# Performance work log

Measured on AMD Instinct MI355X. Metric: run time of the kernel, lower is better.

Reference implementation:

```python
import jax, jax.numpy as jnp
import numpy as np

N_NODES = 100000
N_EDGES = 1600000
N_FEATS = 64
HID1 = 128
HID2 = 128


def setup_inputs() -> dict:
    key = jax.random.key(0)
    ks = jax.random.split(key, 8)
    x = jax.random.normal(ks[0], (N_NODES, N_FEATS), dtype=jnp.float32)
    edge_index = jax.random.randint(ks[1], (2, N_EDGES), 0, N_NODES, dtype=jnp.int64)
    # glorot-ish init for linear weights (out_feats, in_feats), bias zeros (PyG default)
    W1 = jax.random.normal(ks[2], (HID1, N_FEATS), dtype=jnp.float32) * (1.0 / np.sqrt(N_FEATS))
    b1 = jnp.zeros((HID1,), dtype=jnp.float32)
    W2 = jax.random.normal(ks[3], (HID2, HID1), dtype=jnp.float32) * (1.0 / np.sqrt(HID1))
    b2 = jnp.zeros((HID2,), dtype=jnp.float32)
    W3 = jax.random.normal(ks[4], (N_FEATS, HID2), dtype=jnp.float32) * (1.0 / np.sqrt(HID2))
    b3 = jnp.zeros((N_FEATS,), dtype=jnp.float32)
    return {"x": x, "edge_index": edge_index, "W1": W1, "b1": b1,
            "W2": W2, "b2": b2, "W3": W3, "b3": b3}


def _gcn_conv(x, src, dst, norm, W, b, n_nodes):
    # dense linear transform first (out_dim may differ from in_dim)
    h = x @ W.T                                   # [N, out]
    msg = h[src] * norm[:, None]                  # gather + edge-normalize, [E+N, out]
    out = jax.ops.segment_sum(msg, dst, num_segments=n_nodes)  # scatter-add
    return out + b


def reference(x, edge_index, W1, b1, W2, b2, W3, b3):
    n = x.shape[0]
    loop = jnp.arange(n, dtype=edge_index.dtype)
    src = jnp.concatenate([edge_index[0], loop])  # self-loops appended (PyG default)
    dst = jnp.concatenate([edge_index[1], loop])
    # symmetric normalization: deg over target column incl. self-loops
    deg = jax.ops.segment_sum(jnp.ones(dst.shape, dtype=x.dtype), dst, num_segments=n)
    dinv = jnp.where(deg > 0, jax.lax.rsqrt(deg), 0.0)
    norm = dinv[src] * dinv[dst]                  # [E+N]

    h = jax.nn.relu(_gcn_conv(x, src, dst, norm, W1, b1, n))
    h = jax.nn.relu(_gcn_conv(h, src, dst, norm, W2, b2, n))
    h = _gcn_conv(h, src, dst, norm, W3, b3, n)
    return jax.nn.softmax(h, axis=1)
```

## Files before the change

kernel.cpp:

```cpp
#include <hip/hip_runtime.h>
#include <hip/hip_bf16.h>


#define NB1 256

typedef __attribute__((ext_vector_type(4))) _Float16 half4;
typedef __attribute__((ext_vector_type(8))) _Float16 half8;
typedef __attribute__((ext_vector_type(4))) float f32x4;


__global__ __launch_bounds__(256) void k_hist(const int* __restrict__ dst, int E, int C,
                                              int NBUK, int* __restrict__ gh) {
  __shared__ int h[512];
  int t = threadIdx.x, b = blockIdx.x;
  for (int i = t; i < NBUK; i += 256) h[i] = 0;
  __syncthreads();
  int beg = b * C, end = min(beg + C, E);
  for (int i = beg + t; i < end; i += 256) atomicAdd(&h[dst[i] >> 8], 1);
  __syncthreads();
  for (int i = t; i < NBUK; i += 256) gh[i * NB1 + b] = h[i];
}

__global__ __launch_bounds__(256) void k_sum256(const int* __restrict__ g, int L,
                                                int* __restrict__ part) {
  __shared__ int red[256];
  int t = threadIdx.x;
  int idx = blockIdx.x * 256 + t;
  red[t] = (idx < L) ? g[idx] : 0;
  __syncthreads();
  for (int off = 128; off > 0; off >>= 1) {
    if (t < off) red[t] += red[t + off];
    __syncthreads();
  }
  if (t == 0) part[blockIdx.x] = red[0];
}

__global__ __launch_bounds__(512) void k_scan_part(int* __restrict__ part, int NP) {
  __shared__ int sh[512];
  int t = threadIdx.x;
  int v = (t < NP) ? part[t] : 0;
  sh[t] = v;
  __syncthreads();
  for (int off = 1; off < 512; off <<= 1) {
    int u = (t >= off) ? sh[t - off] : 0;
    __syncthreads();
    sh[t] += u;
    __syncthreads();
  }
  if (t < NP) part[t] = sh[t] - v;
}

__global__ __launch_bounds__(256) void k_scan_apply(const int* __restrict__ g, int L,
                                                    const int* __restrict__ part,
                                                    int* __restrict__ gout) {
  __shared__ int sh[256];
  int t = threadIdx.x;
  int idx = blockIdx.x * 256 + t;
  int v = (idx < L) ? g[idx] : 0;
  sh[t] = v;
  __syncthreads();
  for (int off = 1; off < 256; off <<= 1) {
    int u = (t >= off) ? sh[t - off] : 0;
    __syncthreads();
    sh[t] += u;
    __syncthreads();
  }
  if (idx < L) gout[idx] = part[blockIdx.x] + sh[t] - v;
}

__global__ __launch_bounds__(256) void k_scatter(const int* __restrict__ src,
                                                 const int* __restrict__ dst, int E, int C,
                                                 int NBUK, const int* __restrict__ gscan,
                                                 int* __restrict__ epak) {
  __shared__ int cur[512];
  int t = threadIdx.x, b = blockIdx.x;
  for (int i = t; i < NBUK; i += 256) cur[i] = gscan[i * NB1 + b];
  __syncthreads();
  int beg = b * C, end = min(beg + C, E);
  for (int i = beg + t; i < end; i += 256) {
    int d = dst[i];
    int p = atomicAdd(&cur[d >> 8], 1);
    epak[p] = src[i] | ((d & 255) << 24);
  }
}

__global__ __launch_bounds__(256) void k_csr(const int* __restrict__ epak,
                                             const int* __restrict__ gscan, int NBUK, int N, int E,
                                             int* __restrict__ rowptr, float* __restrict__ dinv,
                                             int* __restrict__ col) {
  __shared__ int cnt[256];
  __shared__ int scn[256];
  __shared__ int cur[256];
  int b = blockIdx.x, t = threadIdx.x;
  int ebeg = gscan[b * NB1];
  int eend = (b + 1 < NBUK) ? gscan[(b + 1) * NB1] : E;
  cnt[t] = 0;
  __syncthreads();
  for (int i = ebeg + t; i < eend; i += 256) atomicAdd(&cnt[(epak[i] >> 24) & 255], 1);
  __syncthreads();
  int c = cnt[t];
  scn[t] = c;
  __syncthreads();
  for (int off = 1; off < 256; off <<= 1) {
    int v = (t >= off) ? scn[t - off] : 0;
    __syncthreads();
    scn[t] += v;
    __syncthreads();
  }
  int excl = scn[t] - c;
  int node = b * 256 + t;
  if (node < N) {
    rowptr[node] = ebeg + excl;
    dinv[node] = rsqrtf((float)(c + 1));
  }
  cur[t] = ebeg + excl;
  __syncthreads();
  for (int i = ebeg + t; i < eend; i += 256) {
    int e = epak[i];
    int p = atomicAdd(&cur[(e >> 24) & 255], 1);
    col[p] = e & 0xFFFFFF;
  }
  if (b == 0 && t == 0) rowptr[N] = E;
}

__global__ __launch_bounds__(256) void k_prep_w(const float* __restrict__ W1,
                                                const float* __restrict__ W2,
                                                const float* __restrict__ W3,
                                                _Float16* __restrict__ w1h,
                                                _Float16* __restrict__ w2h,
                                                _Float16* __restrict__ w3h) {
  int i = blockIdx.x * 256 + threadIdx.x;
  if (i < 128 * 64) w1h[i] = (_Float16)W1[i];
  if (i < 128 * 128) w2h[i] = (_Float16)W2[i];
  if (i < 64 * 128) w3h[i] = (_Float16)W3[i];
}

__global__ __launch_bounds__(256) void k_prescaleh(const float* __restrict__ x,
                                                   const float* __restrict__ dinv,
                                                   _Float16* __restrict__ xp, int N) {
  int i = blockIdx.x * 256 + threadIdx.x;
  if (i < N * 16) {
    int row = i >> 4;
    float4 v = ((const float4*)x)[i];
    float d = dinv[row];
    half4 o;
    o[0] = (_Float16)(v.x * d);
    o[1] = (_Float16)(v.y * d);
    o[2] = (_Float16)(v.z * d);
    o[3] = (_Float16)(v.w * d);
    ((half4*)xp)[i] = o;
  }
}


template <int EPI>
__global__ __launch_bounds__(256) void k_agg64h(const _Float16* __restrict__ hp,
                                                const float* __restrict__ dinv,
                                                const int* __restrict__ rowptr,
                                                const int* __restrict__ col,
                                                const float* __restrict__ bias,
                                                void* __restrict__ outp, int N) {
  int wid = blockIdx.x * 4 + (threadIdx.x >> 6);
  int lane = threadIdx.x & 63;
  if (wid >= N) return;
  int g = lane >> 3;
  int fl = (lane & 7) * 8;
  float acc[8] = {0.f, 0.f, 0.f, 0.f, 0.f, 0.f, 0.f, 0.f};
  int r0 = rowptr[wid], r1 = rowptr[wid + 1];
  for (int base = r0; base < r1; base += 64) {
    int mm = min(64, r1 - base);
    int ce = (base + lane < r1) ? col[base + lane] : 0;
    for (int j = 0; j < mm; j += 16) {
      int i0 = j + g, i1 = j + 8 + g;
      int s0 = __shfl(ce, i0);
      int s1 = __shfl(ce, i1);
      if (i0 < mm) {
        half8 v = *(const half8*)&hp[(size_t)s0 * 64 + fl];
#pragma unroll
        for (int k = 0; k < 8; ++k) acc[k] += (float)v[k];
      }
      if (i1 < mm) {
        half8 v = *(const half8*)&hp[(size_t)s1 * 64 + fl];
#pragma unroll
        for (int k = 0; k < 8; ++k) acc[k] += (float)v[k];
      }
    }
  }
#pragma unroll
  for (int o = 8; o < 64; o <<= 1) {
#pragma unroll
    for (int k = 0; k < 8; ++k) acc[k] += __shfl_xor(acc[k], o);
  }
  half8 sv = *(const half8*)&hp[(size_t)wid * 64 + fl];
  float di = dinv[wid];
  float v[8];
#pragma unroll
  for (int k = 0; k < 8; ++k) v[k] = di * (acc[k] + (float)sv[k]);
  if (EPI == 0) {
    if (lane < 8) {
      half8 o;
#pragma unroll
      for (int k = 0; k < 8; ++k) o[k] = (_Float16)v[k];
      *(half8*)&((_Float16*)outp)[(size_t)wid * 64 + fl] = o;
    }
  } else {
    float4 ba = *(const float4*)&bias[fl];
    float4 bb = *(const float4*)&bias[fl + 4];
    v[0] += ba.x; v[1] += ba.y; v[2] += ba.z; v[3] += ba.w;
    v[4] += bb.x; v[5] += bb.y; v[6] += bb.z; v[7] += bb.w;
    float mx = v[0];
#pragma unroll
    for (int k = 1; k < 8; ++k) mx = fmaxf(mx, v[k]);
#pragma unroll
    for (int o = 1; o < 8; o <<= 1) mx = fmaxf(mx, __shfl_xor(mx, o));
    float s = 0.f;
#pragma unroll
    for (int k = 0; k < 8; ++k) {
      v[k] = expf(v[k] - mx);
      s += v[k];
    }
#pragma unroll
    for (int o = 1; o < 8; o <<= 1) s += __shfl_xor(s, o);
    float inv = 1.0f / s;
#pragma unroll
    for (int k = 0; k < 8; ++k) v[k] *= inv;
    if (lane < 8) {
      float4 o0 = make_float4(v[0], v[1], v[2], v[3]);
      float4 o1 = make_float4(v[4], v[5], v[6], v[7]);
      *(float4*)&((float*)outp)[(size_t)wid * 64 + fl] = o0;
      *(float4*)&((float*)outp)[(size_t)wid * 64 + fl + 4] = o1;
    }
  }
}

__global__ __launch_bounds__(256) void k_agg128h(const _Float16* __restrict__ hp,
                                                 const float* __restrict__ dinv,
                                                 const int* __restrict__ rowptr,
                                                 const int* __restrict__ col,
                                                 _Float16* __restrict__ out, int N) {
  int wid = blockIdx.x * 4 + (threadIdx.x >> 6);
  int lane = threadIdx.x & 63;
  if (wid >= N) return;
  int g = lane >> 4;
  int fl = (lane & 15) * 8;
  float acc[8] = {0.f, 0.f, 0.f, 0.f, 0.f, 0.f, 0.f, 0.f};
  int r0 = rowptr[wid], r1 = rowptr[wid + 1];
  for (int base = r0; base < r1; base += 64) {
    int mm = min(64, r1 - base);
    int ce = (base + lane < r1) ? col[base + lane] : 0;
    for (int j = 0; j < mm; j += 8) {
      int i0 = j + g, i1 = j + 4 + g;
      int s0 = __shfl(ce, i0);
      int s1 = __shfl(ce, i1);
      if (i0 < mm) {
        half8 v = *(const half8*)&hp[(size_t)s0 * 128 + fl];
#pragma unroll
        for (int k = 0; k < 8; ++k) acc[k] += (float)v[k];
      }
      if (i1 < mm) {
        half8 v = *(const half8*)&hp[(size_t)s1 * 128 + fl];
#pragma unroll
        for (int k = 0; k < 8; ++k) acc[k] += (float)v[k];
      }
    }
  }
#pragma unroll
  for (int o = 16; o < 64; o <<= 1) {
#pragma unroll
    for (int k = 0; k < 8; ++k) acc[k] += __shfl_xor(acc[k], o);
  }
  half8 sv = *(const half8*)&hp[(size_t)wid * 128 + fl];
  float di = dinv[wid];
  if (lane < 16) {
    half8 o;
#pragma unroll
    for (int k = 0; k < 8; ++k) o[k] = (_Float16)(di * (acc[k] + (float)sv[k]));
    *(half8*)&out[(size_t)wid * 128 + fl] = o;
  }
}


__global__ __launch_bounds__(256) void k_mfma1(const _Float16* __restrict__ a1h,
                                               const _Float16* __restrict__ w1h,
                                               const float* __restrict__ b1,
                                               const float* __restrict__ dinv,
                                               _Float16* __restrict__ h1, int N) {
  int wave = threadIdx.x >> 6, lane = threadIdx.x & 63;
  int rb = blockIdx.x * 128 + wave * 32;
  if (rb >= N) return;
  int lrow = lane & 15, lg = lane >> 4;

  half8 arow[2][2];
#pragma unroll
  for (int rt = 0; rt < 2; ++rt) {
    int r = rb + rt * 16 + lrow;
    if (r >= N) r = N - 1;
    const _Float16* p = &a1h[(size_t)r * 64 + lg * 8];
    arow[rt][0] = *(const half8*)p;
    arow[rt][1] = *(const half8*)(p + 32);
  }
  f32x4 acc[2][8];
#pragma unroll
  for (int rt = 0; rt < 2; ++rt)
#pragma unroll
    for (int nt = 0; nt < 8; ++nt) acc[rt][nt] = (f32x4){0.f, 0.f, 0.f, 0.f};

#pragma unroll
  for (int nt = 0; nt < 8; ++nt) {
#pragma unroll
    for (int ks = 0; ks < 2; ++ks) {
      half8 wf = *(const half8*)&w1h[(size_t)(nt * 16 + lrow) * 64 + ks * 32 + lg * 8];
      acc[0][nt] = __builtin_amdgcn_mfma_f32_16x16x32_f16(wf, arow[0][ks], acc[0][nt], 0, 0, 0);
      acc[1][nt] = __builtin_amdgcn_mfma_f32_16x16x32_f16(wf, arow[1][ks], acc[1][nt], 0, 0, 0);
    }
  }
#pragma unroll
  for (int rt = 0; rt < 2; ++rt) {
    int r = rb + rt * 16 + lrow;
    if (r < N) {
      float di = dinv[r];
#pragma unroll
      for (int nt = 0; nt < 8; ++nt) {
        int n = nt * 16 + lg * 4;
        float4 bb = *(const float4*)&b1[n];
        half4 o;
        o[0] = (_Float16)(fmaxf(acc[rt][nt][0] + bb.x, 0.f) * di);
        o[1] = (_Float16)(fmaxf(acc[rt][nt][1] + bb.y, 0.f) * di);
        o[2] = (_Float16)(fmaxf(acc[rt][nt][2] + bb.z, 0.f) * di);
        o[3] = (_Float16)(fmaxf(acc[rt][nt][3] + bb.w, 0.f) * di);
        *(half4*)&h1[(size_t)r * 128 + n] = o;
      }
    }
  }
}

__global__ __launch_bounds__(256) void k_mfma23(const _Float16* __restrict__ a2h,
                                                const _Float16* __restrict__ w2h,
                                                const float* __restrict__ b2,
                                                const _Float16* __restrict__ w3h,
                                                const float* __restrict__ dinv,
                                                _Float16* __restrict__ hz, int N) {
  __shared__ _Float16 u_lds[4][32][136];
  int wave = threadIdx.x >> 6, lane = threadIdx.x & 63;
  int rb = blockIdx.x * 128 + wave * 32;
  if (rb >= N) return;
  int lrow = lane & 15, lg = lane >> 4;

  half8 frag[2][4];
#pragma unroll
  for (int rt = 0; rt < 2; ++rt) {
    int r = rb + rt * 16 + lrow;
    if (r >= N) r = N - 1;
    const _Float16* p = &a2h[(size_t)r * 128 + lg * 8];
#pragma unroll
    for (int ks = 0; ks < 4; ++ks) frag[rt][ks] = *(const half8*)(p + ks * 32);
  }
  f32x4 acc[2][8];
#pragma unroll
  for (int rt = 0; rt < 2; ++rt)
#pragma unroll
    for (int nt = 0; nt < 8; ++nt) acc[rt][nt] = (f32x4){0.f, 0.f, 0.f, 0.f};

#pragma unroll
  for (int nt = 0; nt < 8; ++nt) {
#pragma unroll
    for (int ks = 0; ks < 4; ++ks) {
      half8 wf = *(const half8*)&w2h[(size_t)(nt * 16 + lrow) * 128 + ks * 32 + lg * 8];
      acc[0][nt] = __builtin_amdgcn_mfma_f32_16x16x32_f16(wf, frag[0][ks], acc[0][nt], 0, 0, 0);
      acc[1][nt] = __builtin_amdgcn_mfma_f32_16x16x32_f16(wf, frag[1][ks], acc[1][nt], 0, 0, 0);
    }
  }
#pragma unroll
  for (int rt = 0; rt < 2; ++rt) {
#pragma unroll
    for (int nt = 0; nt < 8; ++nt) {
      int n = nt * 16 + lg * 4;
      float4 bb = *(const float4*)&b2[n];
      half4 o;
      o[0] = (_Float16)fmaxf(acc[rt][nt][0] + bb.x, 0.f);
      o[1] = (_Float16)fmaxf(acc[rt][nt][1] + bb.y, 0.f);
      o[2] = (_Float16)fmaxf(acc[rt][nt][2] + bb.z, 0.f);
      o[3] = (_Float16)fmaxf(acc[rt][nt][3] + bb.w, 0.f);
      *(half4*)&u_lds[wave][rt * 16 + lrow][n] = o;
    }
  }
#pragma unroll
  for (int rt = 0; rt < 2; ++rt)
#pragma unroll
    for (int ks = 0; ks < 4; ++ks)
      frag[rt][ks] = *(const half8*)&u_lds[wave][rt * 16 + lrow][ks * 32 + lg * 8];

  f32x4 acc2[2][4];
#pragma unroll
  for (int rt = 0; rt < 2; ++rt)
#pragma unroll
    for (int mt = 0; mt < 4; ++mt) acc2[rt][mt] = (f32x4){0.f, 0.f, 0.f, 0.f};

#pragma unroll
  for (int mt = 0; mt < 4; ++mt) {
#pragma unroll
    for (int ks = 0; ks < 4; ++ks) {
      half8 wf = *(const half8*)&w3h[(size_t)(mt * 16 + lrow) * 128 + ks * 32 + lg * 8];
      acc2[0][mt] = __builtin_amdgcn_mfma_f32_16x16x32_f16(wf, frag[0][ks], acc2[0][mt], 0, 0, 0);
      acc2[1][mt] = __builtin_amdgcn_mfma_f32_16x16x32_f16(wf, frag[1][ks], acc2[1][mt], 0, 0, 0);
    }
  }
#pragma unroll
  for (int rt = 0; rt < 2; ++rt) {
    int r = rb + rt * 16 + lrow;
    if (r < N) {
      float di = dinv[r];
#pragma unroll
      for (int mt = 0; mt < 4; ++mt) {
        int m = mt * 16 + lg * 4;
        half4 o;
        o[0] = (_Float16)(acc2[rt][mt][0] * di);
        o[1] = (_Float16)(acc2[rt][mt][1] * di);
        o[2] = (_Float16)(acc2[rt][mt][2] * di);
        o[3] = (_Float16)(acc2[rt][mt][3] * di);
        *(half4*)&hz[(size_t)r * 64 + m] = o;
      }
    }
  }
}


extern "C" void kernel_launch(void* const* d_in, const int* in_sizes, int n_in,
                              void* d_out, int out_size, void* d_ws, size_t ws_size,
                              hipStream_t stream) {
  const float* x  = (const float*)d_in[0];
  const int*   ei = (const int*)d_in[1];
  const float* W1 = (const float*)d_in[2];
  const float* b1 = (const float*)d_in[3];
  const float* W2 = (const float*)d_in[4];
  const float* b2 = (const float*)d_in[5];
  const float* W3 = (const float*)d_in[6];
  const float* b3 = (const float*)d_in[7];
  float* out = (float*)d_out;

  const int N = in_sizes[0] / 64;
  const int E = in_sizes[1] / 2;
  const int* esrc = ei;
  const int* edst = ei + E;

  const int NBUK = (N + 255) / 256;
  const int C1 = (E + NB1 - 1) / NB1;
  const int L = NBUK * NB1;
  const int NA = (L + 255) / 256;

  char* w = (char*)d_ws;
  auto take = [&](size_t bytes) -> void* {
    void* p = (void*)w;
    w += (bytes + 255) & ~(size_t)255;
    return p;
  };
  int*   rowptr = (int*)take((size_t)(N + 1) * 4);
  float* dinv   = (float*)take((size_t)N * 4);
  int*   col    = (int*)take((size_t)E * 4);
  int*   gh     = (int*)take((size_t)L * 4);
  int*   gscan  = (int*)take((size_t)L * 4);
  int*   part   = (int*)take((size_t)NA * 4);
  _Float16* w1h = (_Float16*)take((size_t)128 * 64 * 2);
  _Float16* w2h = (_Float16*)take((size_t)128 * 128 * 2);
  _Float16* w3h = (_Float16*)take((size_t)64 * 128 * 2);
  _Float16* hx  = (_Float16*)take((size_t)N * 64 * 2);
  _Float16* a1h = (_Float16*)take((size_t)N * 64 * 2);
  _Float16* h1  = (_Float16*)take((size_t)N * 128 * 2);
  _Float16* a2h = (_Float16*)take((size_t)N * 128 * 2);
  int*   epak   = (int*)h1;
  _Float16* hz  = hx;

  k_hist<<<NB1, 256, 0, stream>>>(edst, E, C1, NBUK, gh);
  k_sum256<<<NA, 256, 0, stream>>>(gh, L, part);
  k_scan_part<<<1, 512, 0, stream>>>(part, NA);
  k_scan_apply<<<NA, 256, 0, stream>>>(gh, L, part, gscan);
  k_scatter<<<NB1, 256, 0, stream>>>(esrc, edst, E, C1, NBUK, gscan, epak);
  k_csr<<<NBUK, 256, 0, stream>>>(epak, gscan, NBUK, N, E, rowptr, dinv, col);

  k_prep_w<<<64, 256, 0, stream>>>(W1, W2, W3, w1h, w2h, w3h);

  const int aggblocks = (N + 3) / 4;
  const int mfmablocks = (N + 127) / 128;

  k_prescaleh<<<(N * 16 + 255) / 256, 256, 0, stream>>>(x, dinv, hx, N);
  k_agg64h<0><<<aggblocks, 256, 0, stream>>>(hx, dinv, rowptr, col, nullptr, a1h, N);
  k_mfma1<<<mfmablocks, 256, 0, stream>>>(a1h, w1h, b1, dinv, h1, N);
  k_agg128h<<<aggblocks, 256, 0, stream>>>(h1, dinv, rowptr, col, a2h, N);
  k_mfma23<<<mfmablocks, 256, 0, stream>>>(a2h, w2h, b2, w3h, dinv, hz, N);
  k_agg64h<1><<<aggblocks, 256, 0, stream>>>(hz, dinv, rowptr, col, b3, out, N);
}
```

Before: 357.6 us.

## Fuse preprocessing kernels and unroll aggregation gathers to four neighbors

Folds the weight fp16 conversion into extra blocks of the histogram kernel, merges the partial-sum scan into the scan-apply kernel, and moves the x prescaling into the CSR build kernel. Together these remove three kernel launches. The aggregation loops now issue four neighbor gathers per step instead of two, to raise memory-level parallelism. The trade-offs are that the fused x prescale does strided per-thread row reads and each scan block redundantly sums the partials.

```diff
diff --git a/kernel.cpp b/kernel.cpp
--- a/kernel.cpp
+++ b/kernel.cpp
@@ -10,9 +10,22 @@
 
 
 __global__ __launch_bounds__(256) void k_hist(const int* __restrict__ dst, int E, int C,
-                                              int NBUK, int* __restrict__ gh) {
+                                              int NBUK, int* __restrict__ gh,
+                                              const float* __restrict__ W1,
+                                              const float* __restrict__ W2,
+                                              const float* __restrict__ W3,
+                                              _Float16* __restrict__ w1h,
+                                              _Float16* __restrict__ w2h,
+                                              _Float16* __restrict__ w3h) {
+  int t = threadIdx.x, b = blockIdx.x;
+  if (b >= NB1) {
+    int i = (b - NB1) * 256 + t;
+    if (i < 128 * 64) w1h[i] = (_Float16)W1[i];
+    if (i < 128 * 128) w2h[i] = (_Float16)W2[i];
+    if (i < 64 * 128) w3h[i] = (_Float16)W3[i];
+    return;
+  }
   __shared__ int h[512];
-  int t = threadIdx.x, b = blockIdx.x;
   for (int i = t; i < NBUK; i += 256) h[i] = 0;
   __syncthreads();
   int beg = b * C, end = min(beg + C, E);
@@ -35,27 +48,26 @@
   if (t == 0) part[blockIdx.x] = red[0];
 }
 
-__global__ __launch_bounds__(512) void k_scan_part(int* __restrict__ part, int NP) {
-  __shared__ int sh[512];
-  int t = threadIdx.x;
-  int v = (t < NP) ? part[t] : 0;
-  sh[t] = v;
-  __syncthreads();
-  for (int off = 1; off < 512; off <<= 1) {
-    int u = (t >= off) ? sh[t - off] : 0;
+__global__ __launch_bounds__(256) void k_scan_apply(const int* __restrict__ g, int L,
+                                                    const int* __restrict__ part, int NP,
+                                                    int* __restrict__ gout) {
+  __shared__ int pl[512];
+  __shared__ int sh[256];
+  int t = threadIdx.x, bid = blockIdx.x;
+  pl[t] = (t < NP) ? part[t] : 0;
+  pl[t + 256] = (t + 256 < NP) ? part[t + 256] : 0;
+  __syncthreads();
+  int partial = 0;
+  for (int i = t; i < bid; i += 256) partial += pl[i];
+  sh[t] = partial;
+  __syncthreads();
+  for (int off = 128; off > 0; off >>= 1) {
+    if (t < off) sh[t] += sh[t + off];
     __syncthreads();
-    sh[t] += u;
-    __syncthreads();
-  }
-  if (t < NP) part[t] = sh[t] - v;
-}
-
-__global__ __launch_bounds__(256) void k_scan_apply(const int* __restrict__ g, int L,
-                                                    const int* __restrict__ part,
-                                                    int* __restrict__ gout) {
-  __shared__ int sh[256];
-  int t = threadIdx.x;
-  int idx = blockIdx.x * 256 + t;
+  }
+  int pre = sh[0];
+  __syncthreads();
+  int idx = bid * 256 + t;
   int v = (idx < L) ? g[idx] : 0;
   sh[t] = v;
   __syncthreads();
@@ -65,7 +77,7 @@
     sh[t] += u;
     __syncthreads();
   }
-  if (idx < L) gout[idx] = part[blockIdx.x] + sh[t] - v;
+  if (idx < L) gout[idx] = pre + sh[t] - v;
 }
 
 __global__ __launch_bounds__(256) void k_scatter(const int* __restrict__ src,
@@ -87,7 +99,9 @@
 __global__ __launch_bounds__(256) void k_csr(const int* __restrict__ epak,
                                              const int* __restrict__ gscan, int NBUK, int N, int E,
                                              int* __restrict__ rowptr, float* __restrict__ dinv,
-                                             int* __restrict__ col) {
+                                             int* __restrict__ col,
+                                             const float* __restrict__ x,
+                                             _Float16* __restrict__ hx) {
   __shared__ int cnt[256];
   __shared__ int scn[256];
   __shared__ int cur[256];
@@ -109,9 +123,10 @@
   }
   int excl = scn[t] - c;
   int node = b * 256 + t;
+  float d = rsqrtf((float)(c + 1));
   if (node < N) {
     rowptr[node] = ebeg + excl;
-    dinv[node] = rsqrtf((float)(c + 1));
+    dinv[node] = d;
   }
   cur[t] = ebeg + excl;
   __syncthreads();
@@ -121,34 +136,19 @@
     col[p] = e & 0xFFFFFF;
   }
   if (b == 0 && t == 0) rowptr[N] = E;
-}
-
-__global__ __launch_bounds__(256) void k_prep_w(const float* __restrict__ W1,
-                                                const float* __restrict__ W2,
-                                                const float* __restrict__ W3,
-                                                _Float16* __restrict__ w1h,
-                                                _Float16* __restrict__ w2h,
-                                                _Float16* __restrict__ w3h) {
-  int i = blockIdx.x * 256 + threadIdx.x;
-  if (i < 128 * 64) w1h[i] = (_Float16)W1[i];
-  if (i < 128 * 128) w2h[i] = (_Float16)W2[i];
-  if (i < 64 * 128) w3h[i] = (_Float16)W3[i];
-}
-
-__global__ __launch_bounds__(256) void k_prescaleh(const float* __restrict__ x,
-                                                   const float* __restrict__ dinv,
-                                                   _Float16* __restrict__ xp, int N) {
-  int i = blockIdx.x * 256 + threadIdx.x;
-  if (i < N * 16) {
-    int row = i >> 4;
-    float4 v = ((const float4*)x)[i];
-    float d = dinv[row];
-    half4 o;
-    o[0] = (_Float16)(v.x * d);
-    o[1] = (_Float16)(v.y * d);
-    o[2] = (_Float16)(v.z * d);
-    o[3] = (_Float16)(v.w * d);
-    ((half4*)xp)[i] = o;
+  if (node < N) {
+    const float4* xr = (const float4*)&x[(size_t)node * 64];
+    half8* hr = (half8*)&hx[(size_t)node * 64];
+#pragma unroll
+    for (int q = 0; q < 8; ++q) {
+      float4 a = xr[q * 2], bb = xr[q * 2 + 1];
+      half8 o;
+      o[0] = (_Float16)(a.x * d); o[1] = (_Float16)(a.y * d);
+      o[2] = (_Float16)(a.z * d); o[3] = (_Float16)(a.w * d);
+      o[4] = (_Float16)(bb.x * d); o[5] = (_Float16)(bb.y * d);
+      o[6] = (_Float16)(bb.z * d); o[7] = (_Float16)(bb.w * d);
+      hr[q] = o;
+    }
   }
 }
 
@@ -170,10 +170,10 @@
   for (int base = r0; base < r1; base += 64) {
     int mm = min(64, r1 - base);
     int ce = (base + lane < r1) ? col[base + lane] : 0;
-    for (int j = 0; j < mm; j += 16) {
-      int i0 = j + g, i1 = j + 8 + g;
-      int s0 = __shfl(ce, i0);
-      int s1 = __shfl(ce, i1);
+    for (int j = 0; j < mm; j += 32) {
+      int i0 = j + g, i1 = j + 8 + g, i2 = j + 16 + g, i3 = j + 24 + g;
+      int s0 = __shfl(ce, i0), s1 = __shfl(ce, i1);
+      int s2 = __shfl(ce, i2), s3 = __shfl(ce, i3);
       if (i0 < mm) {
         half8 v = *(const half8*)&hp[(size_t)s0 * 64 + fl];
 #pragma unroll
@@ -181,6 +181,16 @@
       }
       if (i1 < mm) {
         half8 v = *(const half8*)&hp[(size_t)s1 * 64 + fl];
+#pragma unroll
+        for (int k = 0; k < 8; ++k) acc[k] += (float)v[k];
+      }
+      if (i2 < mm) {
+        half8 v = *(const half8*)&hp[(size_t)s2 * 64 + fl];
+#pragma unroll
+        for (int k = 0; k < 8; ++k) acc[k] += (float)v[k];
+      }
+      if (i3 < mm) {
+        half8 v = *(const half8*)&hp[(size_t)s3 * 64 + fl];
 #pragma unroll
         for (int k = 0; k < 8; ++k) acc[k] += (float)v[k];
       }
@@ -248,10 +258,10 @@
   for (int base = r0; base < r1; base += 64) {
     int mm = min(64, r1 - base);
     int ce = (base + lane < r1) ? col[base + lane] : 0;
-    for (int j = 0; j < mm; j += 8) {
-      int i0 = j + g, i1 = j + 4 + g;
-      int s0 = __shfl(ce, i0);
-      int s1 = __shfl(ce, i1);
+    for (int j = 0; j < mm; j += 16) {
+      int i0 = j + g, i1 = j + 4 + g, i2 = j + 8 + g, i3 = j + 12 + g;
+      int s0 = __shfl(ce, i0), s1 = __shfl(ce, i1);
+      int s2 = __shfl(ce, i2), s3 = __shfl(ce, i3);
       if (i0 < mm) {
         half8 v = *(const half8*)&hp[(size_t)s0 * 128 + fl];
 #pragma unroll
@@ -259,6 +269,16 @@
       }
       if (i1 < mm) {
         half8 v = *(const half8*)&hp[(size_t)s1 * 128 + fl];
+#pragma unroll
+        for (int k = 0; k < 8; ++k) acc[k] += (float)v[k];
+      }
+      if (i2 < mm) {
+        half8 v = *(const half8*)&hp[(size_t)s2 * 128 + fl];
+#pragma unroll
+        for (int k = 0; k < 8; ++k) acc[k] += (float)v[k];
+      }
+      if (i3 < mm) {
+        half8 v = *(const half8*)&hp[(size_t)s3 * 128 + fl];
 #pragma unroll
         for (int k = 0; k < 8; ++k) acc[k] += (float)v[k];
       }
@@ -470,19 +490,15 @@
   int*   epak   = (int*)h1;
   _Float16* hz  = hx;
 
-  k_hist<<<NB1, 256, 0, stream>>>(edst, E, C1, NBUK, gh);
+  k_hist<<<NB1 + 128, 256, 0, stream>>>(edst, E, C1, NBUK, gh, W1, W2, W3, w1h, w2h, w3h);
   k_sum256<<<NA, 256, 0, stream>>>(gh, L, part);
-  k_scan_part<<<1, 512, 0, stream>>>(part, NA);
-  k_scan_apply<<<NA, 256, 0, stream>>>(gh, L, part, gscan);
+  k_scan_apply<<<NA, 256, 0, stream>>>(gh, L, part, NA, gscan);
   k_scatter<<<NB1, 256, 0, stream>>>(esrc, edst, E, C1, NBUK, gscan, epak);
-  k_csr<<<NBUK, 256, 0, stream>>>(epak, gscan, NBUK, N, E, rowptr, dinv, col);
-
-  k_prep_w<<<64, 256, 0, stream>>>(W1, W2, W3, w1h, w2h, w3h);
+  k_csr<<<NBUK, 256, 0, stream>>>(epak, gscan, NBUK, N, E, rowptr, dinv, col, x, hx);
 
   const int aggblocks = (N + 3) / 4;
   const int mfmablocks = (N + 127) / 128;
 
-  k_prescaleh<<<(N * 16 + 255) / 256, 256, 0, stream>>>(x, dinv, hx, N);
   k_agg64h<0><<<aggblocks, 256, 0, stream>>>(hx, dinv, rowptr, col, nullptr, a1h, N);
   k_mfma1<<<mfmablocks, 256, 0, stream>>>(a1h, w1h, b1, dinv, h1, N);
   k_agg128h<<<aggblocks, 256, 0, stream>>>(h1, dinv, rowptr, col, a2h, N);
```

New measurement: 358.7 us. Within noise of the previous version (+0.3%).
